# Optimization experiments

Hardware: AMD Instinct MI355X
Metric: run time of the kernel (lower is better)

The kernel has to match this reference:

```python
import math
import jax, jax.numpy as jnp
import numpy as np
from jax import lax

FEATURE_DIM = 1024
EMBED_DIM = 300
VOCAB = 32000
HIDDEN = 512
BATCH = 64
MAX_LEN = 40
S = 3  # number of feature maps summed in l_total


def setup_inputs() -> dict:
    key = jax.random.key(0)
    ks = jax.random.split(key, 10)
    l_total = jax.random.normal(ks[0], (S, BATCH, FEATURE_DIM), jnp.float32)
    encoded_captions = jax.random.randint(ks[1], (BATCH, MAX_LEN), 0, VOCAB)
    lengths = jax.random.randint(ks[2], (BATCH,), 5, MAX_LEN + 1)
    lengths = lengths.at[0].set(MAX_LEN)  # ensure max(decode_lengths) == MAX_LEN-1 (static)
    caption_lengths = lengths[:, None]
    # parameters (per PlainDecoder.init_weights / torch defaults)
    emb_weight = jax.random.uniform(ks[3], (VOCAB, EMBED_DIM), jnp.float32, -0.1, 0.1)
    k = 1.0 / math.sqrt(HIDDEN)
    W_ih = jax.random.uniform(ks[4], (4 * HIDDEN, EMBED_DIM + FEATURE_DIM), jnp.float32, -k, k)
    W_hh = jax.random.uniform(ks[5], (4 * HIDDEN, HIDDEN), jnp.float32, -k, k)
    b_ih = jax.random.uniform(ks[6], (4 * HIDDEN,), jnp.float32, -k, k)
    b_hh = jax.random.uniform(ks[7], (4 * HIDDEN,), jnp.float32, -k, k)
    wdc_W = jax.random.uniform(ks[8], (VOCAB, HIDDEN), jnp.float32, -0.1, 0.1)
    wdc_b = jnp.zeros((VOCAB,), jnp.float32)
    return {
        "l_total": l_total,
        "encoded_captions": encoded_captions,
        "caption_lengths": caption_lengths,
        "emb_weight": emb_weight,
        "W_ih": W_ih,
        "W_hh": W_hh,
        "b_ih": b_ih,
        "b_hh": b_hh,
        "wdc_W": wdc_W,
        "wdc_b": wdc_b,
    }


def reference(l_total, encoded_captions, caption_lengths, emb_weight, W_ih, W_hh, b_ih, b_hh, wdc_W, wdc_b):
    # l_total: (S, B, F) -> permute(1,2,0).sum(-1) -> (B, F)
    lt = jnp.transpose(l_total, (1, 2, 0)).sum(-1)
    lengths = caption_lengths[:, 0]
    sort_ind = jnp.argsort(-lengths)  # descending
    lengths_s = lengths[sort_ind]
    lt = lt[sort_ind]
    caps = encoded_captions[sort_ind]
    decode_lengths = lengths_s - 1
    embeds = emb_weight[caps]  # (B, L, E)

    T = caps.shape[1] - 1  # static max decode length (max length pinned in setup)
    B = caps.shape[0]
    H = W_hh.shape[1]

    emb_seq = jnp.transpose(embeds[:, :T, :], (1, 0, 2))  # (T, B, E)
    mask = jnp.arange(T)[:, None] < decode_lengths[None, :]  # (T, B)

    def step(carry, xs):
        h, c = carry
        emb_t, mask_t = xs
        x = jnp.concatenate([emb_t, lt], axis=1)  # (B, E+F)
        gates = x @ W_ih.T + h @ W_hh.T + b_ih + b_hh  # (B, 4H)
        i, f, g, o = jnp.split(gates, 4, axis=1)  # torch gate order: i,f,g,o
        i = jax.nn.sigmoid(i)
        f = jax.nn.sigmoid(f)
        g = jnp.tanh(g)
        o = jax.nn.sigmoid(o)
        c = f * c + i * g
        h = o * jnp.tanh(c)
        pred = h @ wdc_W.T + wdc_b  # (B, V)
        pred = jnp.where(mask_t[:, None], pred, jnp.zeros((), pred.dtype))
        return (h, c), pred

    h0 = jnp.zeros((B, H), lt.dtype)
    c0 = jnp.zeros((B, H), lt.dtype)
    _, preds = lax.scan(step, (h0, c0), (emb_seq, mask))  # (T, B, V)
    predictions = jnp.transpose(preds, (1, 0, 2))  # (B, T, V)
    return predictions, caps, decode_lengths, sort_ind
```

## Files before the change

### kernel.cpp

```cpp
#include <hip/hip_runtime.h>
#include <hip/hip_bf16.h>
#include <math.h>

typedef float f32x4 __attribute__((ext_vector_type(4)));
typedef __bf16 bf16x8 __attribute__((ext_vector_type(8)));
typedef __bf16 bf16x4 __attribute__((ext_vector_type(4)));
typedef unsigned long long u64;

#define BATCH   64
#define TSTEPS  39
#define HID     512
#define GATES   2048
#define NVOCAB  32000
#define EMBD    300
#define FEAT    1024
#define XDIM    1324

#define PRED_ELEMS (BATCH*TSTEPS*NVOCAB)

#define WS_CNT     0
#define WS_SORT    256
#define WS_DECLEN  512
#define WS_CAPS    1024
#define WS_LT      65536
#define WS_CONST   327680
#define WS_XP      1048576
#define WS_HALL    22020096
#define WS_WDCB    25165824

__device__ __forceinline__ u64 agent_load_u64(const u64* p) {
    return __hip_atomic_load(p, __ATOMIC_RELAXED, __HIP_MEMORY_SCOPE_AGENT);
}
__device__ __forceinline__ void agent_store_u32(unsigned int* p, unsigned int v) {
    __hip_atomic_store(p, v, __ATOMIC_RELAXED, __HIP_MEMORY_SCOPE_AGENT);
}

__global__ void k0_setup(const int* caplen, const int* enc,
                         float* out_caps, float* out_declen, float* out_sort,
                         int* ws_sort, int* ws_declen, int* ws_caps,
                         unsigned int* cnt) {
    __shared__ int L[BATCH];
    __shared__ int sind[BATCH];
    int tid = threadIdx.x;
    if (tid == 0) *cnt = 0u;
    if (tid < BATCH) L[tid] = caplen[tid];
    __syncthreads();
    if (tid < BATCH) {
        int len = L[tid];
        int rank = 0;
        for (int j = 0; j < BATCH; ++j) {
            int lj = L[j];
            if (lj > len || (lj == len && j < tid)) rank++;
        }
        sind[rank] = tid;
    }
    __syncthreads();
    if (tid < BATCH) {
        int src = sind[tid];
        ws_sort[tid] = src;
        int dl = L[src] - 1;
        ws_declen[tid] = dl;
        out_declen[tid] = (float)dl;
        out_sort[tid] = (float)src;
    }
    __syncthreads();
    for (int x = tid; x < BATCH*40; x += blockDim.x) {
        int b = x / 40, t = x % 40;
        int v = enc[sind[b]*40 + t];
        ws_caps[x] = v;
        out_caps[x] = (float)v;
    }
}

__global__ void k1_lt(const float* l_total, const int* ws_sort, float* lt) {
    int b = blockIdx.x;
    int ob = ws_sort[b];
    for (int k4 = threadIdx.x; k4 < FEAT/4; k4 += blockDim.x) {
        float4 a = ((const float4*)(l_total + (0*BATCH + ob)*FEAT))[k4];
        float4 c = ((const float4*)(l_total + (1*BATCH + ob)*FEAT))[k4];
        float4 d = ((const float4*)(l_total + (2*BATCH + ob)*FEAT))[k4];
        float4 r;
        r.x = a.x + c.x + d.x;  r.y = a.y + c.y + d.y;
        r.z = a.z + c.z + d.z;  r.w = a.w + c.w + d.w;
        ((float4*)(lt + b*FEAT))[k4] = r;
    }
}

__global__ void k2_const(const float* W_ih, const float* lt,
                         const float* b_ih, const float* b_hh, float* cst) {
    __shared__ float As[32][68];
    __shared__ float Bs[32][36];
    int ctile = blockIdx.x;
    int btile = blockIdx.y;
    int tid = threadIdx.x;
    int ty = tid >> 4, tx = tid & 15;
    float acc[4][2] = {};
    for (int kc = 0; kc < 32; ++kc) {
        __syncthreads();
        #pragma unroll
        for (int j = 0; j < 8; ++j) {
            int idx = tid + j*256;
            int c = idx >> 5, k = idx & 31;
            As[k][c] = W_ih[(ctile*64 + c)*XDIM + 300 + kc*32 + k];
        }
        #pragma unroll
        for (int j = 0; j < 4; ++j) {
            int idx = tid + j*256;
            int b = idx >> 5, k = idx & 31;
            Bs[k][b] = lt[(btile*32 + b)*FEAT + kc*32 + k];
        }
        __syncthreads();
        for (int k = 0; k < 32; ++k) {
            float4 av = *(const float4*)&As[k][ty*4];
            float2 bv = *(const float2*)&Bs[k][tx*2];
            acc[0][0] += av.x*bv.x; acc[0][1] += av.x*bv.y;
            acc[1][0] += av.y*bv.x; acc[1][1] += av.y*bv.y;
            acc[2][0] += av.z*bv.x; acc[2][1] += av.z*bv.y;
            acc[3][0] += av.w*bv.x; acc[3][1] += av.w*bv.y;
        }
    }
    #pragma unroll
    for (int i = 0; i < 4; ++i) {
        int cg = ctile*64 + ty*4 + i;
        float bias = b_ih[cg] + b_hh[cg];
        float2 o;
        o.x = acc[i][0] + bias; o.y = acc[i][1] + bias;
        *(float2*)&cst[cg*64 + btile*32 + tx*2] = o;
    }
}

__global__ void k3_xp(const float* W_ih, const float* emb, const int* ws_caps,
                      const float* cst, float* Xp) {
    __shared__ float As[20][68];
    __shared__ float Bs[20][68];
    int ctile = blockIdx.x;
    int t = blockIdx.y;
    int tid = threadIdx.x;
    int ty = tid >> 4, tx = tid & 15;
    float acc[4][4] = {};
    for (int kc = 0; kc < 15; ++kc) {
        __syncthreads();
        #pragma unroll
        for (int j = 0; j < 5; ++j) {
            int idx = tid + j*256;
            int c = idx / 20, k = idx % 20;
            As[k][c] = W_ih[(ctile*64 + c)*XDIM + kc*20 + k];
        }
        #pragma unroll
        for (int j = 0; j < 5; ++j) {
            int idx = tid + j*256;
            int b = idx / 20, k = idx % 20;
            int tok = ws_caps[b*40 + t];
            Bs[k][b] = emb[tok*EMBD + kc*20 + k];
        }
        __syncthreads();
        for (int k = 0; k < 20; ++k) {
            float4 av = *(const float4*)&As[k][ty*4];
            float4 bv = *(const float4*)&Bs[k][tx*4];
            acc[0][0] += av.x*bv.x; acc[0][1] += av.x*bv.y; acc[0][2] += av.x*bv.z; acc[0][3] += av.x*bv.w;
            acc[1][0] += av.y*bv.x; acc[1][1] += av.y*bv.y; acc[1][2] += av.y*bv.z; acc[1][3] += av.y*bv.w;
            acc[2][0] += av.z*bv.x; acc[2][1] += av.z*bv.y; acc[2][2] += av.z*bv.z; acc[2][3] += av.z*bv.w;
            acc[3][0] += av.w*bv.x; acc[3][1] += av.w*bv.y; acc[3][2] += av.w*bv.z; acc[3][3] += av.w*bv.w;
        }
    }
    #pragma unroll
    for (int i = 0; i < 4; ++i) {
        int cg = ctile*64 + ty*4 + i;
        float4 cs = *(const float4*)&cst[cg*64 + tx*4];
        float4 o;
        o.x = acc[i][0] + cs.x; o.y = acc[i][1] + cs.y;
        o.z = acc[i][2] + cs.z; o.w = acc[i][3] + cs.w;
        *(float4*)&Xp[(t*GATES + cg)*64 + tx*4] = o;
    }
}

__global__ void k4_cvt(const float* wdc, __bf16* wdcb) {
    int n4 = NVOCAB*HID/4;
    for (int i = blockIdx.x*blockDim.x + threadIdx.x; i < n4; i += gridDim.x*blockDim.x) {
        float4 v = ((const float4*)wdc)[i];
        bf16x4 o;
        o[0] = (__bf16)v.x; o[1] = (__bf16)v.y; o[2] = (__bf16)v.z; o[3] = (__bf16)v.w;
        ((bf16x4*)wdcb)[i] = o;
    }
}

__global__ void __launch_bounds__(256) k5_lstm(const float* W_hh, const float* Xp,
                                               __bf16* h_all, unsigned int* cnt) {
    __shared__ float gates_lds[32][64];
    __shared__ float c_lds[8][64];
    __shared__ __bf16 h_s[64][8];
    int p = blockIdx.x;
    int tid = threadIdx.x;
    int l = tid & 63, w = tid >> 6;

    bf16x8 wfrag[2][16];
    #pragma unroll
    for (int mt = 0; mt < 2; ++mt) {
        int rr = mt*16 + (l & 15);
        int grow = (rr >> 3)*HID + p*8 + (rr & 7);
        const float* wrow = W_hh + grow*HID;
        #pragma unroll
        for (int kc = 0; kc < 16; ++kc) {
            int k0 = kc*32 + (l >> 4)*8;
            float4 f0 = *(const float4*)(wrow + k0);
            float4 f1 = *(const float4*)(wrow + k0 + 4);
            bf16x8 v;
            v[0]=(__bf16)f0.x; v[1]=(__bf16)f0.y; v[2]=(__bf16)f0.z; v[3]=(__bf16)f0.w;
            v[4]=(__bf16)f1.x; v[5]=(__bf16)f1.y; v[6]=(__bf16)f1.z; v[7]=(__bf16)f1.w;
            wfrag[mt][kc] = v;
        }
    }
    for (int x = tid; x < 8*64; x += 256) ((float*)c_lds)[x] = 0.0f;
    __syncthreads();

    int ulA = tid >> 6;
    int bA  = tid & 63;

    for (int t = 0; t < TSTEPS; ++t) {
        float xg[2][4];
        {
            const float* xpt = Xp + (size_t)t*GATES*64;
            int u0 = p*8 + ulA;
            #pragma unroll
            for (int g = 0; g < 4; ++g) {
                xg[0][g] = xpt[((size_t)g*512 + u0    )*64 + bA];
                xg[1][g] = xpt[((size_t)g*512 + u0 + 4)*64 + bA];
            }
        }

        if (t == 0) {
            for (int x = tid; x < 32*64; x += 256) ((float*)gates_lds)[x] = 0.0f;
        } else {
            f32x4 acc0 = {0.f,0.f,0.f,0.f};
            f32x4 acc1 = {0.f,0.f,0.f,0.f};
            int bb = w*16 + (l & 15);
            const u64* hq = (const u64*)(h_all + (size_t)(t-1)*BATCH*HID + bb*HID + (l >> 4)*8);
            u64 hl[16][2];
            #pragma unroll
            for (int kc = 0; kc < 16; ++kc) {
                hl[kc][0] = agent_load_u64(hq + kc*4);
                hl[kc][1] = agent_load_u64(hq + kc*4 + 1);
            }
            #pragma unroll
            for (int kc = 0; kc < 16; ++kc) {
                union { bf16x8 v; u64 u[2]; } uu;
                uu.u[0] = hl[kc][0]; uu.u[1] = hl[kc][1];
                acc0 = __builtin_amdgcn_mfma_f32_16x16x32_bf16(wfrag[0][kc], uu.v, acc0, 0, 0, 0);
                acc1 = __builtin_amdgcn_mfma_f32_16x16x32_bf16(wfrag[1][kc], uu.v, acc1, 0, 0, 0);
            }
            #pragma unroll
            for (int j = 0; j < 4; ++j) {
                gates_lds[(l>>4)*4 + j][bb]      = acc0[j];
                gates_lds[16 + (l>>4)*4 + j][bb] = acc1[j];
            }
        }
        __syncthreads();

        #pragma unroll
        for (int half = 0; half < 2; ++half) {
            int ul = ulA + half*4;
            int b  = bA;
            float gi = gates_lds[ul][b]      + xg[half][0];
            float gf = gates_lds[8+ul][b]    + xg[half][1];
            float gg = gates_lds[16+ul][b]   + xg[half][2];
            float go = gates_lds[24+ul][b]   + xg[half][3];
            float ig = 1.0f/(1.0f + expf(-gi));
            float fg = 1.0f/(1.0f + expf(-gf));
            float gv = tanhf(gg);
            float og = 1.0f/(1.0f + expf(-go));
            float c = fg * c_lds[ul][b] + ig * gv;
            c_lds[ul][b] = c;
            float h = og * tanhf(c);
            h_s[b][ul] = (__bf16)h;
        }
        __syncthreads();

        {
            int row = tid >> 2, seg = tid & 3;
            unsigned int val = ((const unsigned int*)&h_s[0][0])[row*4 + seg];
            unsigned int* dst = (unsigned int*)(h_all + ((size_t)t*BATCH + row)*HID + p*8);
            agent_store_u32(dst + seg, val);
        }

        if (t < TSTEPS - 1) {
            __syncthreads();
            if (tid == 0) {
                __hip_atomic_fetch_add(cnt, 1u, __ATOMIC_RELAXED, __HIP_MEMORY_SCOPE_AGENT);
                unsigned int target = (unsigned int)(t + 1) * gridDim.x;
                while (__hip_atomic_load(cnt, __ATOMIC_RELAXED, __HIP_MEMORY_SCOPE_AGENT) < target) {
                    __builtin_amdgcn_s_sleep(2);
                }
            }
            __syncthreads();
        }
    }
}

__global__ void __launch_bounds__(256) k6_pred(const __bf16* h_all, const __bf16* wdcb,
                                               const float* wdc_b, const int* ws_declen,
                                               float* out) {
    __shared__ __bf16 As[128][40];
    __shared__ __bf16 Bs[128][40];
    int mtile = blockIdx.x;
    int ntile = blockIdx.y;
    int tid = threadIdx.x;
    int l = tid & 63, w = tid >> 6;
    int wm = w >> 1, wn = w & 1;

    f32x4 acc[4][4];
    #pragma unroll
    for (int i = 0; i < 4; ++i)
        #pragma unroll
        for (int j = 0; j < 4; ++j)
            acc[i][j] = (f32x4){0.f,0.f,0.f,0.f};

    for (int kc = 0; kc < 16; ++kc) {
        __syncthreads();
        #pragma unroll
        for (int j = 0; j < 2; ++j) {
            int idx = tid + j*256;
            int row = idx >> 2, seg = idx & 3;
            int rg = mtile*128 + row;
            bf16x8 v;
            if (rg < TSTEPS*BATCH) {
                v = *(const bf16x8*)(h_all + (size_t)rg*HID + kc*32 + seg*8);
            } else {
                #pragma unroll
                for (int q = 0; q < 8; ++q) v[q] = (__bf16)0.0f;
            }
            *(bf16x8*)&As[row][seg*8] = v;
            int cg = ntile*128 + row;
            *(bf16x8*)&Bs[row][seg*8] = *(const bf16x8*)(wdcb + (size_t)cg*HID + kc*32 + seg*8);
        }
        __syncthreads();
        bf16x8 af[4], bf[4];
        #pragma unroll
        for (int s = 0; s < 4; ++s) {
            af[s] = *(const bf16x8*)&As[wm*64 + s*16 + (l & 15)][(l >> 4)*8];
            bf[s] = *(const bf16x8*)&Bs[wn*64 + s*16 + (l & 15)][(l >> 4)*8];
        }
        #pragma unroll
        for (int sm = 0; sm < 4; ++sm)
            #pragma unroll
            for (int sn = 0; sn < 4; ++sn)
                acc[sm][sn] = __builtin_amdgcn_mfma_f32_16x16x32_bf16(af[sm], bf[sn], acc[sm][sn], 0, 0, 0);
    }

    #pragma unroll
    for (int sm = 0; sm < 4; ++sm) {
        #pragma unroll
        for (int j = 0; j < 4; ++j) {
            int R = mtile*128 + wm*64 + sm*16 + (l >> 4)*4 + j;
            if (R >= TSTEPS*BATCH) continue;
            int t = R >> 6, b = R & 63;
            int dl = ws_declen[b];
            #pragma unroll
            for (int sn = 0; sn < 4; ++sn) {
                int C = ntile*128 + wn*64 + sn*16 + (l & 15);
                float v = (t < dl) ? (acc[sm][sn][j] + wdc_b[C]) : 0.0f;
                out[((size_t)b*TSTEPS + t)*NVOCAB + C] = v;
            }
        }
    }
}

extern "C" void kernel_launch(void* const* d_in, const int* in_sizes, int n_in,
                              void* d_out, int out_size, void* d_ws, size_t ws_size,
                              hipStream_t stream) {
    const float* l_total = (const float*)d_in[0];
    const int*   enc     = (const int*)d_in[1];
    const int*   caplen  = (const int*)d_in[2];
    const float* emb     = (const float*)d_in[3];
    const float* W_ih    = (const float*)d_in[4];
    const float* W_hh    = (const float*)d_in[5];
    const float* b_ih    = (const float*)d_in[6];
    const float* b_hh    = (const float*)d_in[7];
    const float* wdc_W   = (const float*)d_in[8];
    const float* wdc_b   = (const float*)d_in[9];

    float* out = (float*)d_out;
    char* ws = (char*)d_ws;

    unsigned int* cnt   = (unsigned int*)(ws + WS_CNT);
    int* ws_sort        = (int*)(ws + WS_SORT);
    int* ws_declen      = (int*)(ws + WS_DECLEN);
    int* ws_caps        = (int*)(ws + WS_CAPS);
    float* lt           = (float*)(ws + WS_LT);
    float* cst          = (float*)(ws + WS_CONST);
    float* Xp           = (float*)(ws + WS_XP);
    __bf16* h_all       = (__bf16*)(ws + WS_HALL);
    __bf16* wdcb        = (__bf16*)(ws + WS_WDCB);

    float* out_caps   = out + PRED_ELEMS;
    float* out_declen = out_caps + BATCH*40;
    float* out_sort   = out_declen + BATCH;

    k0_setup<<<1, 256, 0, stream>>>(caplen, enc, out_caps, out_declen, out_sort,
                                    ws_sort, ws_declen, ws_caps, cnt);
    k1_lt<<<BATCH, 256, 0, stream>>>(l_total, ws_sort, lt);
    k2_const<<<dim3(32, 2), 256, 0, stream>>>(W_ih, lt, b_ih, b_hh, cst);
    k3_xp<<<dim3(32, TSTEPS), 256, 0, stream>>>(W_ih, emb, ws_caps, cst, Xp);
    k4_cvt<<<2048, 256, 0, stream>>>(wdc_W, wdcb);
    k5_lstm<<<64, 256, 0, stream>>>(W_hh, Xp, h_all, cnt);
    k6_pred<<<dim3(20, NVOCAB/128), 256, 0, stream>>>(h_all, wdcb, wdc_b, ws_declen, out);
}
```

Baseline: 916.9 us.

## Replace LSTM grid-wide barrier with sentinel-based per-element dataflow polling

The atomic-counter grid barrier between LSTM timesteps is removed. Instead, the conversion kernel pre-fills the hidden-state buffer with 0xFFFFFFFF sentinel words. Each block then re-polls its h loads until no sentinel words remain, so a block waits only for the data it actually needs rather than for every block in the grid. The h read stride per k-chunk also changes from 4 to 8 u64, which looks like an indexing fix. The costs are an extra 2.5 MB sentinel fill and a reliance on relaxed agent-scope loads seeing the other blocks' stores.

```diff
diff --git a/kernel.cpp b/kernel.cpp
--- a/kernel.cpp
+++ b/kernel.cpp
@@ -5,6 +5,7 @@
 typedef float f32x4 __attribute__((ext_vector_type(4)));
 typedef __bf16 bf16x8 __attribute__((ext_vector_type(8)));
 typedef __bf16 bf16x4 __attribute__((ext_vector_type(4)));
+typedef unsigned int u32x4 __attribute__((ext_vector_type(4)));
 typedef unsigned long long u64;
 
 #define BATCH   64
@@ -37,12 +38,10 @@
 
 __global__ void k0_setup(const int* caplen, const int* enc,
                          float* out_caps, float* out_declen, float* out_sort,
-                         int* ws_sort, int* ws_declen, int* ws_caps,
-                         unsigned int* cnt) {
+                         int* ws_sort, int* ws_declen, int* ws_caps) {
     __shared__ int L[BATCH];
     __shared__ int sind[BATCH];
     int tid = threadIdx.x;
-    if (tid == 0) *cnt = 0u;
     if (tid < BATCH) L[tid] = caplen[tid];
     __syncthreads();
     if (tid < BATCH) {
@@ -174,18 +173,23 @@
     }
 }
 
-__global__ void k4_cvt(const float* wdc, __bf16* wdcb) {
+__global__ void k4_cvt(const float* wdc, __bf16* wdcb, u32x4* hsent) {
+    int gid = blockIdx.x*blockDim.x + threadIdx.x;
+    int stride = gridDim.x*blockDim.x;
     int n4 = NVOCAB*HID/4;
-    for (int i = blockIdx.x*blockDim.x + threadIdx.x; i < n4; i += gridDim.x*blockDim.x) {
+    for (int i = gid; i < n4; i += stride) {
         float4 v = ((const float4*)wdc)[i];
         bf16x4 o;
         o[0] = (__bf16)v.x; o[1] = (__bf16)v.y; o[2] = (__bf16)v.z; o[3] = (__bf16)v.w;
         ((bf16x4*)wdcb)[i] = o;
     }
+    int nh16 = TSTEPS*BATCH*HID*2/16;
+    u32x4 s = {0xFFFFFFFFu, 0xFFFFFFFFu, 0xFFFFFFFFu, 0xFFFFFFFFu};
+    for (int i = gid; i < nh16; i += stride) hsent[i] = s;
 }
 
 __global__ void __launch_bounds__(256) k5_lstm(const float* W_hh, const float* Xp,
-                                               __bf16* h_all, unsigned int* cnt) {
+                                               __bf16* h_all) {
     __shared__ float gates_lds[32][64];
     __shared__ float c_lds[8][64];
     __shared__ __bf16 h_s[64][8];
@@ -231,16 +235,32 @@
         if (t == 0) {
             for (int x = tid; x < 32*64; x += 256) ((float*)gates_lds)[x] = 0.0f;
         } else {
-            f32x4 acc0 = {0.f,0.f,0.f,0.f};
-            f32x4 acc1 = {0.f,0.f,0.f,0.f};
             int bb = w*16 + (l & 15);
             const u64* hq = (const u64*)(h_all + (size_t)(t-1)*BATCH*HID + bb*HID + (l >> 4)*8);
             u64 hl[16][2];
             #pragma unroll
             for (int kc = 0; kc < 16; ++kc) {
-                hl[kc][0] = agent_load_u64(hq + kc*4);
-                hl[kc][1] = agent_load_u64(hq + kc*4 + 1);
-            }
+                hl[kc][0] = agent_load_u64(hq + kc*8);
+                hl[kc][1] = agent_load_u64(hq + kc*8 + 1);
+            }
+            bool dirty = true;
+            while (dirty) {
+                dirty = false;
+                #pragma unroll
+                for (int kc = 0; kc < 16; ++kc) {
+                    #pragma unroll
+                    for (int j = 0; j < 2; ++j) {
+                        u64 v = hl[kc][j];
+                        if ((unsigned int)v == 0xFFFFFFFFu ||
+                            (unsigned int)(v >> 32) == 0xFFFFFFFFu) {
+                            hl[kc][j] = agent_load_u64(hq + kc*8 + j);
+                            dirty = true;
+                        }
+                    }
+                }
+            }
+            f32x4 acc0 = {0.f,0.f,0.f,0.f};
+            f32x4 acc1 = {0.f,0.f,0.f,0.f};
             #pragma unroll
             for (int kc = 0; kc < 16; ++kc) {
                 union { bf16x8 v; u64 u[2]; } uu;
@@ -281,18 +301,6 @@
             unsigned int* dst = (unsigned int*)(h_all + ((size_t)t*BATCH + row)*HID + p*8);
             agent_store_u32(dst + seg, val);
         }
-
-        if (t < TSTEPS - 1) {
-            __syncthreads();
-            if (tid == 0) {
-                __hip_atomic_fetch_add(cnt, 1u, __ATOMIC_RELAXED, __HIP_MEMORY_SCOPE_AGENT);
-                unsigned int target = (unsigned int)(t + 1) * gridDim.x;
-                while (__hip_atomic_load(cnt, __ATOMIC_RELAXED, __HIP_MEMORY_SCOPE_AGENT) < target) {
-                    __builtin_amdgcn_s_sleep(2);
-                }
-            }
-            __syncthreads();
-        }
     }
 }
 
@@ -381,7 +389,6 @@
     float* out = (float*)d_out;
     char* ws = (char*)d_ws;
 
-    unsigned int* cnt   = (unsigned int*)(ws + WS_CNT);
     int* ws_sort        = (int*)(ws + WS_SORT);
     int* ws_declen      = (int*)(ws + WS_DECLEN);
     int* ws_caps        = (int*)(ws + WS_CAPS);
@@ -396,11 +403,11 @@
     float* out_sort   = out_declen + BATCH;
 
     k0_setup<<<1, 256, 0, stream>>>(caplen, enc, out_caps, out_declen, out_sort,
-                                    ws_sort, ws_declen, ws_caps, cnt);
+                                    ws_sort, ws_declen, ws_caps);
     k1_lt<<<BATCH, 256, 0, stream>>>(l_total, ws_sort, lt);
     k2_const<<<dim3(32, 2), 256, 0, stream>>>(W_ih, lt, b_ih, b_hh, cst);
     k3_xp<<<dim3(32, TSTEPS), 256, 0, stream>>>(W_ih, emb, ws_caps, cst, Xp);
-    k4_cvt<<<2048, 256, 0, stream>>>(wdc_W, wdcb);
-    k5_lstm<<<64, 256, 0, stream>>>(W_hh, Xp, h_all, cnt);
+    k4_cvt<<<2048, 256, 0, stream>>>(wdc_W, wdcb, (u32x4*)h_all);
+    k5_lstm<<<64, 256, 0, stream>>>(W_hh, Xp, h_all);
     k6_pred<<<dim3(20, NVOCAB/128), 256, 0, stream>>>(h_all, wdcb, wdc_b, ws_declen, out);
 }
```

New measurement: 952.5 us. 1.04x slower.
